# Kernel tuning notes

Hardware: AMD Instinct MI355X
Metric: run time of the kernel (lower is better)

## Reference

```python
import jax, jax.numpy as jnp
import numpy as np

NUM_HEADS = 16
HEAD_DIM = 64  # hidden_size 1024 / 16 heads


def setup_inputs() -> dict:
    key = jax.random.key(0)
    ks = jax.random.split(key, 7)
    B, S, D = 32, 577, 1024
    s = 0.02
    return {
        "hidden_states": jax.random.normal(ks[0], (B, S, D), dtype=jnp.float32),
        "Wq": jax.random.normal(ks[1], (D, D), dtype=jnp.float32) * s,
        "bq": jax.random.normal(ks[2], (D,), dtype=jnp.float32) * s,
        "Wk": jax.random.normal(ks[3], (D, D), dtype=jnp.float32) * s,
        "bk": jax.random.normal(ks[4], (D,), dtype=jnp.float32) * s,
        "Wv": jax.random.normal(ks[5], (D, D), dtype=jnp.float32) * s,
        "bv": jax.random.normal(ks[6], (D,), dtype=jnp.float32) * s,
    }


def _split_heads(x):
    # [B, S, D] -> [B, H, S, d]
    B, S, D = x.shape
    return x.reshape(B, S, NUM_HEADS, HEAD_DIM).transpose(0, 2, 1, 3)


def reference(hidden_states, Wq, bq, Wk, bk, Wv, bv):
    # torch Linear: y = x @ W^T + b
    q = _split_heads(hidden_states @ Wq.T + bq)  # [B,H,S,d]
    k = _split_heads(hidden_states @ Wk.T + bk)
    v = _split_heads(hidden_states @ Wv.T + bv)

    scale = 1.0 / np.sqrt(HEAD_DIM).astype(np.float32)
    scores = jnp.einsum("bhqd,bhkd->bhqk", q, k) * scale  # [B,H,S,S]
    probs = jax.nn.softmax(scores, axis=-1)
    ctx = jnp.einsum("bhqk,bhkd->bhqd", probs, v)  # [B,H,S,d]
    B, H, S, d = ctx.shape
    ctx = ctx.transpose(0, 2, 1, 3).reshape(B, S, H * d)  # [B,S,D]
    return ctx
```

## Files before the change

kernel.cpp:

```cpp
#include <hip/hip_runtime.h>
#include <stdint.h>

#define NB 32
#define SEQ 577
#define SPAD 640
#define NH 16
#define HD 64
#define DM 1024
#define MTOT (NB * SEQ)

typedef __bf16 bf16x8 __attribute__((ext_vector_type(8)));
typedef float f32x4 __attribute__((ext_vector_type(4)));
typedef unsigned short u16x8 __attribute__((ext_vector_type(8)));
typedef unsigned short u16x4 __attribute__((ext_vector_type(4)));

__device__ __forceinline__ unsigned short f2bf(float f) {
  unsigned int u = __builtin_bit_cast(unsigned int, f);
  return (unsigned short)((u + 0x7FFFu + ((u >> 16) & 1u)) >> 16);
}

__device__ __forceinline__ f32x4 mfma16(bf16x8 a, bf16x8 b, f32x4 c) {
  return __builtin_amdgcn_mfma_f32_16x16x32_bf16(a, b, c, 0, 0, 0);
}

__device__ __forceinline__ void gload16(const unsigned short* g, unsigned short* l) {
  __builtin_amdgcn_global_load_lds(
      (const __attribute__((address_space(1))) unsigned int*)g,
      (__attribute__((address_space(3))) unsigned int*)l, 16, 0, 0);
}

#if __has_builtin(__builtin_amdgcn_exp2f)
#define EXP2(x) __builtin_amdgcn_exp2f(x)
#else
#define EXP2(x) exp2f(x)
#endif

__global__ void cvt_kernel(const float* __restrict__ x,
                           const float* __restrict__ wq,
                           const float* __restrict__ wk,
                           const float* __restrict__ wv,
                           unsigned short* __restrict__ xb,
                           unsigned short* __restrict__ wb) {
  const long long NX = (long long)MTOT * DM;
  long long i = ((long long)blockIdx.x * blockDim.x + threadIdx.x) * 4;
  const float* src;
  unsigned short* dst;
  if (i < NX) {
    src = x + i;
    dst = xb + i;
  } else {
    long long j = i - NX;
    int wsel = (int)(j >> 20);
    long long off = j & 0xFFFFF;
    src = (wsel == 0 ? wq : wsel == 1 ? wk : wv) + off;
    dst = wb + j;
  }
  f32x4 v = *(const f32x4*)src;
  u16x4 o;
  o.x = f2bf(v.x); o.y = f2bf(v.y); o.z = f2bf(v.z); o.w = f2bf(v.w);
  *(u16x4*)dst = o;
}

__global__ __launch_bounds__(256, 2) void qkv_gemm(
    const unsigned short* __restrict__ xb, const unsigned short* __restrict__ wb,
    const float* __restrict__ bq, const float* __restrict__ bk,
    const float* __restrict__ bv, unsigned short* __restrict__ qo,
    unsigned short* __restrict__ ko, unsigned short* __restrict__ vo) {
  __shared__ __align__(16) unsigned short As[128 * 32];
  __shared__ __align__(16) unsigned short Bs[128 * 32];
  const int t = threadIdx.x;
  const int z = blockIdx.z;
  const int m0 = blockIdx.y * 128;
  const int n0 = blockIdx.x * 128;
  const unsigned short* W = wb + (size_t)z * (DM * DM);
  const float* bias = (z == 0 ? bq : z == 1 ? bk : bv);

  const int lane = t & 63;
  const int g = lane >> 4, c = lane & 15;
  const int w = t >> 6;
  const int wm = w & 1, wn = w >> 1;

  const int srow = t >> 2;
  const int scol = (t & 3) * 8;
  int ar0 = m0 + srow;      if (ar0 > MTOT - 1) ar0 = MTOT - 1;
  int ar1 = m0 + 64 + srow; if (ar1 > MTOT - 1) ar1 = MTOT - 1;
  const unsigned short* gA0 = xb + (size_t)ar0 * DM + scol;
  const unsigned short* gA1 = xb + (size_t)ar1 * DM + scol;
  const unsigned short* gB0 = W + (size_t)(n0 + srow) * DM + scol;
  const unsigned short* gB1 = W + (size_t)(n0 + 64 + srow) * DM + scol;
  unsigned short* lA0 = As + t * 8;
  unsigned short* lA1 = As + 2048 + t * 8;
  unsigned short* lB0 = Bs + t * 8;
  unsigned short* lB1 = Bs + 2048 + t * 8;

  f32x4 acc[4][4];
#pragma unroll
  for (int mi = 0; mi < 4; mi++)
#pragma unroll
    for (int ni = 0; ni < 4; ni++) acc[mi][ni] = (f32x4)0.0f;

  for (int k0 = 0; k0 < DM; k0 += 32) {
    __syncthreads();
    gload16(gA0 + k0, lA0);
    gload16(gA1 + k0, lA1);
    gload16(gB0 + k0, lB0);
    gload16(gB1 + k0, lB1);
    __syncthreads();
    bf16x8 af[4], bfr[4];
#pragma unroll
    for (int mi = 0; mi < 4; mi++)
      af[mi] = __builtin_bit_cast(
          bf16x8, *(const u16x8*)(As + (wm * 64 + mi * 16 + c) * 32 + g * 8));
#pragma unroll
    for (int ni = 0; ni < 4; ni++)
      bfr[ni] = __builtin_bit_cast(
          bf16x8, *(const u16x8*)(Bs + (wn * 64 + ni * 16 + c) * 32 + g * 8));
#pragma unroll
    for (int mi = 0; mi < 4; mi++)
#pragma unroll
      for (int ni = 0; ni < 4; ni++)
        acc[mi][ni] = mfma16(af[mi], bfr[ni], acc[mi][ni]);
  }

  float bias4[4];
#pragma unroll
  for (int ni = 0; ni < 4; ni++) bias4[ni] = bias[n0 + wn * 64 + ni * 16 + c];

#pragma unroll
  for (int mi = 0; mi < 4; mi++) {
    int mb = m0 + wm * 64 + mi * 16 + g * 4;
#pragma unroll
    for (int r = 0; r < 4; r++) {
      int m = mb + r;
      if (m >= MTOT) continue;
      int bi = m / SEQ;
      int s = m - bi * SEQ;
#pragma unroll
      for (int ni = 0; ni < 4; ni++) {
        int n = n0 + wn * 64 + ni * 16 + c;
        int hh = n >> 6, dd = n & 63;
        unsigned short v = f2bf(acc[mi][ni][r] + bias4[ni]);
        if (z == 2)
          vo[(((size_t)bi * NH + hh) * HD + dd) * SPAD + s] = v;
        else if (z == 0)
          qo[(((size_t)bi * NH + hh) * SPAD + s) * HD + dd] = v;
        else
          ko[(((size_t)bi * NH + hh) * SPAD + s) * HD + dd] = v;
      }
    }
  }
}

__global__ __launch_bounds__(256, 4) void attn_kernel(
    const unsigned short* __restrict__ Qb, const unsigned short* __restrict__ Kb,
    const unsigned short* __restrict__ Vt, float* __restrict__ out) {
  __shared__ __align__(16) unsigned short Ks[64 * 64];
  __shared__ __align__(16) unsigned short Vs[80 * 64];
  __shared__ __align__(16) unsigned short Pl[4][16 * 72];
  const int t = threadIdx.x, lane = t & 63, w = t >> 6;
  const int g = lane >> 4, c = lane & 15;
  const int qt = blockIdx.x, h = blockIdx.y, b = blockIdx.z;
  const int q0 = qt * 64 + w * 16;
  const size_t bh = (size_t)b * NH + h;
  const unsigned short* Qp = Qb + bh * SPAD * HD;
  const unsigned short* Kp = Kb + bh * SPAD * HD;
  const unsigned short* Vp = Vt + bh * HD * SPAD;

  {
    int rr = t >> 4, col = (t & 15) * 4;
    unsigned short val = (rr == 0) ? (unsigned short)0x3F80 : (unsigned short)0;
    u16x4 v4 = {val, val, val, val};
    *(u16x4*)(Vs + (64 + rr) * 64 + col) = v4;
  }

  bf16x8 qf0 = __builtin_bit_cast(
      bf16x8, *(const u16x8*)(Qp + (size_t)(q0 + c) * HD + g * 8));
  bf16x8 qf1 = __builtin_bit_cast(
      bf16x8, *(const u16x8*)(Qp + (size_t)(q0 + c) * HD + 32 + g * 8));

  const int C0 = t, C1 = t + 256;
  const int r0 = C0 >> 3, cg0 = (C0 & 7) ^ (r0 & 7);
  const int r1 = C1 >> 3, cg1 = (C1 & 7) ^ (r1 & 7);
  const unsigned short* gK0 = Kp + (size_t)(r0 * 8 + cg0) * 8;
  const unsigned short* gK1 = Kp + (size_t)(r1 * 8 + cg1) * 8;
  const unsigned short* gV0 = Vp + (size_t)r0 * SPAD + cg0 * 8;
  const unsigned short* gV1 = Vp + (size_t)r1 * SPAD + cg1 * 8;
  unsigned short* lK0 = Ks + C0 * 8;
  unsigned short* lK1 = Ks + C1 * 8;
  unsigned short* lV0 = Vs + C0 * 8;
  unsigned short* lV1 = Vs + C1 * 8;

  f32x4 oacc[5];
#pragma unroll
  for (int nt = 0; nt < 5; nt++) oacc[nt] = (f32x4)0.0f;
  unsigned short* pl = &Pl[w][0];
  const float SC = 0.125f * 1.44269504f;

  for (int kt = 0; kt < 10; kt++) {
    const int kv0 = kt * 64;
    __syncthreads();
    gload16(gK0 + kv0 * 64, lK0);
    gload16(gK1 + kv0 * 64, lK1);
    gload16(gV0 + kv0, lV0);
    gload16(gV1 + kv0, lV1);
    __syncthreads();

    f32x4 sc[4];
#pragma unroll
    for (int nt = 0; nt < 4; nt++) {
      const int row = nt * 16 + c;
      const unsigned short* kb = Ks + row * 64;
      bf16x8 k0 = __builtin_bit_cast(
          bf16x8, *(const u16x8*)(kb + ((g ^ (row & 7)) * 8)));
      bf16x8 k1 = __builtin_bit_cast(
          bf16x8, *(const u16x8*)(kb + (((4 + g) ^ (row & 7)) * 8)));
      sc[nt] = mfma16(qf0, k0, (f32x4)0.0f);
      sc[nt] = mfma16(qf1, k1, sc[nt]);
    }

    if (kt == 9) {
#pragma unroll
      for (int nt = 0; nt < 4; nt++) {
        const bool valid = (kv0 + nt * 16 + c) < SEQ;
#pragma unroll
        for (int r = 0; r < 4; r++)
          sc[nt][r] = valid ? EXP2(sc[nt][r] * SC) : 0.0f;
      }
    } else {
#pragma unroll
      for (int nt = 0; nt < 4; nt++)
#pragma unroll
        for (int r = 0; r < 4; r++) sc[nt][r] = EXP2(sc[nt][r] * SC);
    }

#pragma unroll
    for (int nt = 0; nt < 4; nt++)
#pragma unroll
      for (int r = 0; r < 4; r++)
        pl[(g * 4 + r) * 72 + nt * 16 + c] = f2bf(sc[nt][r]);
    bf16x8 pa0 = __builtin_bit_cast(bf16x8, *(const u16x8*)(pl + c * 72 + g * 8));
    bf16x8 pa1 =
        __builtin_bit_cast(bf16x8, *(const u16x8*)(pl + c * 72 + 32 + g * 8));

#pragma unroll
    for (int nt = 0; nt < 5; nt++) {
      const int row = nt * 16 + c;
      const unsigned short* vb = Vs + row * 64;
      bf16x8 v0 = __builtin_bit_cast(
          bf16x8, *(const u16x8*)(vb + ((g ^ (row & 7)) * 8)));
      bf16x8 v1 = __builtin_bit_cast(
          bf16x8, *(const u16x8*)(vb + (((4 + g) ^ (row & 7)) * 8)));
      oacc[nt] = mfma16(pa0, v0, oacc[nt]);
      oacc[nt] = mfma16(pa1, v1, oacc[nt]);
    }
  }

#pragma unroll
  for (int r = 0; r < 4; r++) {
    int s = q0 + g * 4 + r;
    if (s >= SEQ) continue;
    float l = __shfl(oacc[4][r], lane & 48, 64);
    float inv = 1.0f / l;
#pragma unroll
    for (int nt = 0; nt < 4; nt++)
      out[((size_t)b * SEQ + s) * DM + h * HD + nt * 16 + c] =
          oacc[nt][r] * inv;
  }
}

extern "C" void kernel_launch(void* const* d_in, const int* in_sizes, int n_in,
                              void* d_out, int out_size, void* d_ws,
                              size_t ws_size, hipStream_t stream) {
  const float* x = (const float*)d_in[0];
  const float* Wq = (const float*)d_in[1];
  const float* bq = (const float*)d_in[2];
  const float* Wk = (const float*)d_in[3];
  const float* bk = (const float*)d_in[4];
  const float* Wv = (const float*)d_in[5];
  const float* bv = (const float*)d_in[6];
  float* out = (float*)d_out;

  const size_t nXB = (size_t)MTOT * DM;
  const size_t nWB = (size_t)3 * DM * DM;
  const size_t nQK = (size_t)NB * NH * SPAD * HD;
  const size_t needed = (nXB + nWB + 3 * nQK) * 2;
  if (ws_size < needed) return;

  unsigned short* xb = (unsigned short*)d_ws;
  unsigned short* wb = xb + nXB;
  unsigned short* Qb = wb + nWB;
  unsigned short* Kb = Qb + nQK;
  unsigned short* Vt = Kb + nQK;

  cvt_kernel<<<21536, 256, 0, stream>>>(x, Wq, Wk, Wv, xb, wb);
  qkv_gemm<<<dim3(8, 145, 3), 256, 0, stream>>>(xb, wb, bq, bk, bv, Qb, Kb, Vt);
  attn_kernel<<<dim3(10, NH, NB), 256, 0, stream>>>(Qb, Kb, Vt, out);
}
```

Measured before the change: 464.3 us.

## Remap QKV GEMM grid for XCD locality and transpose MFMA for V stores

The 3D launch grid becomes a 1D grid, with block ids remapped so that each XCD (id & 7) handles a fixed set of three weight column tiles. Blocks that reuse the same weight slices then share an L2. For the V projection the MFMA operands are swapped so each lane holds consecutive sequence positions, which is meant to make the transposed V stores less scattered. The grid is padded to 3648 blocks, and the extra blocks exit early.

```diff
diff --git a/kernel.cpp b/kernel.cpp
--- a/kernel.cpp
+++ b/kernel.cpp
@@ -66,12 +66,19 @@
     const float* __restrict__ bq, const float* __restrict__ bk,
     const float* __restrict__ bv, unsigned short* __restrict__ qo,
     unsigned short* __restrict__ ko, unsigned short* __restrict__ vo) {
+  const int id = blockIdx.x;
+  const int xcd = id & 7;
+  const int slot = id >> 3;
+  const int m_tile = slot / 3;
+  if (m_tile >= 145) return;
+  const int nz = xcd * 3 + (slot - m_tile * 3);
+  const int z = nz >> 3;
+  const int n0 = (nz & 7) * 128;
+  const int m0 = m_tile * 128;
+
   __shared__ __align__(16) unsigned short As[128 * 32];
   __shared__ __align__(16) unsigned short Bs[128 * 32];
   const int t = threadIdx.x;
-  const int z = blockIdx.z;
-  const int m0 = blockIdx.y * 128;
-  const int n0 = blockIdx.x * 128;
   const unsigned short* W = wb + (size_t)z * (DM * DM);
   const float* bias = (z == 0 ? bq : z == 1 ? bk : bv);
 
@@ -115,37 +122,63 @@
     for (int ni = 0; ni < 4; ni++)
       bfr[ni] = __builtin_bit_cast(
           bf16x8, *(const u16x8*)(Bs + (wn * 64 + ni * 16 + c) * 32 + g * 8));
-#pragma unroll
-    for (int mi = 0; mi < 4; mi++)
-#pragma unroll
-      for (int ni = 0; ni < 4; ni++)
-        acc[mi][ni] = mfma16(af[mi], bfr[ni], acc[mi][ni]);
-  }
-
-  float bias4[4];
-#pragma unroll
-  for (int ni = 0; ni < 4; ni++) bias4[ni] = bias[n0 + wn * 64 + ni * 16 + c];
-
-#pragma unroll
-  for (int mi = 0; mi < 4; mi++) {
-    int mb = m0 + wm * 64 + mi * 16 + g * 4;
-#pragma unroll
-    for (int r = 0; r < 4; r++) {
-      int m = mb + r;
-      if (m >= MTOT) continue;
-      int bi = m / SEQ;
-      int s = m - bi * SEQ;
-#pragma unroll
-      for (int ni = 0; ni < 4; ni++) {
-        int n = n0 + wn * 64 + ni * 16 + c;
+    if (z == 2) {
+#pragma unroll
+      for (int mi = 0; mi < 4; mi++)
+#pragma unroll
+        for (int ni = 0; ni < 4; ni++)
+          acc[mi][ni] = mfma16(bfr[ni], af[mi], acc[mi][ni]);
+    } else {
+#pragma unroll
+      for (int mi = 0; mi < 4; mi++)
+#pragma unroll
+        for (int ni = 0; ni < 4; ni++)
+          acc[mi][ni] = mfma16(af[mi], bfr[ni], acc[mi][ni]);
+    }
+  }
+
+  if (z == 2) {
+#pragma unroll
+    for (int ni = 0; ni < 4; ni++) {
+#pragma unroll
+      for (int r = 0; r < 4; r++) {
+        int n = n0 + wn * 64 + ni * 16 + g * 4 + r;
         int hh = n >> 6, dd = n & 63;
-        unsigned short v = f2bf(acc[mi][ni][r] + bias4[ni]);
-        if (z == 2)
-          vo[(((size_t)bi * NH + hh) * HD + dd) * SPAD + s] = v;
-        else if (z == 0)
-          qo[(((size_t)bi * NH + hh) * SPAD + s) * HD + dd] = v;
-        else
-          ko[(((size_t)bi * NH + hh) * SPAD + s) * HD + dd] = v;
+        float bn = bias[n];
+#pragma unroll
+        for (int mi = 0; mi < 4; mi++) {
+          int m = m0 + wm * 64 + mi * 16 + c;
+          if (m >= MTOT) continue;
+          int bi = m / SEQ;
+          int s = m - bi * SEQ;
+          vo[(((size_t)bi * NH + hh) * HD + dd) * SPAD + s] =
+              f2bf(acc[mi][ni][r] + bn);
+        }
+      }
+    }
+  } else {
+    float bias4[4];
+#pragma unroll
+    for (int ni = 0; ni < 4; ni++) bias4[ni] = bias[n0 + wn * 64 + ni * 16 + c];
+#pragma unroll
+    for (int mi = 0; mi < 4; mi++) {
+      int mb = m0 + wm * 64 + mi * 16 + g * 4;
+#pragma unroll
+      for (int r = 0; r < 4; r++) {
+        int m = mb + r;
+        if (m >= MTOT) continue;
+        int bi = m / SEQ;
+        int s = m - bi * SEQ;
+#pragma unroll
+        for (int ni = 0; ni < 4; ni++) {
+          int n = n0 + wn * 64 + ni * 16 + c;
+          int hh = n >> 6, dd = n & 63;
+          unsigned short v = f2bf(acc[mi][ni][r] + bias4[ni]);
+          if (z == 0)
+            qo[(((size_t)bi * NH + hh) * SPAD + s) * HD + dd] = v;
+          else
+            ko[(((size_t)bi * NH + hh) * SPAD + s) * HD + dd] = v;
+        }
       }
     }
   }
@@ -293,6 +326,6 @@
   unsigned short* Vt = Kb + nQK;
 
   cvt_kernel<<<21536, 256, 0, stream>>>(x, Wq, Wk, Wv, xb, wb);
-  qkv_gemm<<<dim3(8, 145, 3), 256, 0, stream>>>(xb, wb, bq, bk, bv, Qb, Kb, Vt);
+  qkv_gemm<<<3648, 256, 0, stream>>>(xb, wb, bq, bk, bv, Qb, Kb, Vt);
   attn_kernel<<<dim3(10, NH, NB), 256, 0, stream>>>(Qb, Kb, Vt, out);
 }
```

Measured after the change: 469.7 us. No clear change (+1.2%).
